# Optimization experiments

Measured on AMD Instinct MI355X. Metric: run time of the kernel, lower is better.

The kernel has to match this reference:

```python
import jax, jax.numpy as jnp
import numpy as np

N_NODES = 50000
N_EDGES = 1600000
NFEAT, NHID, NCLASS = 256, 128, 40
DROPOUT_P = 0.5


def gcn_conv(x, W, b, src, dst, n):
    # PyG GCNConv: h = X W; add self-loops; symmetric norm D^-1/2 (A+I) D^-1/2.
    h = x @ W  # [N, out]
    loop = jnp.arange(n, dtype=src.dtype)
    s = jnp.concatenate([src, loop])  # [E+N]
    d = jnp.concatenate([dst, loop])
    deg = jax.ops.segment_sum(jnp.ones_like(d, dtype=h.dtype), d, num_segments=n)  # in-degree incl. self-loop
    dinv = jax.lax.rsqrt(jnp.maximum(deg, 1.0))
    norm = dinv[s] * dinv[d]  # [E+N]
    msg = h[s] * norm[:, None]  # [E+N, out] gather
    out = jax.ops.segment_sum(msg, d, num_segments=n)  # scatter-add
    return out + b


def setup_inputs() -> dict:
    key = jax.random.key(0)
    k = jax.random.split(key, 7)
    x = jax.random.normal(k[0], (N_NODES, NFEAT), dtype=jnp.float32)
    edge_index = jax.random.randint(k[1], (2, N_EDGES), 0, N_NODES, dtype=jnp.int64)
    W1 = jax.random.normal(k[2], (NFEAT, NHID), dtype=jnp.float32) * (1.0 / np.sqrt(NFEAT))
    b1 = jnp.zeros((NHID,), dtype=jnp.float32)
    W2 = jax.random.normal(k[3], (NHID, NCLASS), dtype=jnp.float32) * (1.0 / np.sqrt(NHID))
    b2 = jnp.zeros((NCLASS,), dtype=jnp.float32)
    keep = jax.random.bernoulli(k[4], 1.0 - DROPOUT_P, (N_NODES, NHID))
    drop_mask = keep.astype(jnp.float32) / (1.0 - DROPOUT_P)  # fixed training-mode dropout mask
    return {"x": x, "edge_index": edge_index, "W1": W1, "b1": b1, "W2": W2, "b2": b2, "drop_mask": drop_mask}


def reference(x, edge_index, W1, b1, W2, b2, drop_mask):
    src, dst = edge_index[0], edge_index[1]
    h = gcn_conv(x, W1, b1, src, dst, N_NODES)
    h = jax.nn.relu(h)
    h = h * drop_mask  # F.dropout(training=True) with fixed mask
    h = gcn_conv(h, W2, b2, src, dst, N_NODES)
    return jax.nn.log_softmax(h, axis=1)
```

## Files before the change

kernel.cpp:

```cpp
#include <hip/hip_runtime.h>
#include <hip/hip_fp16.h>
#include <math.h>

#define N_NODES 50000
#define N_EDGES 1600000
#define NFEAT 256
#define NHID 128
#define NCLASS 40

#define BSHIFT 7
#define NBUCK 391
#define CAP 5120
#define EPB 4096

typedef _Float16 f16x8 __attribute__((ext_vector_type(8)));
typedef float f32x4 __attribute__((ext_vector_type(4)));

__global__ __launch_bounds__(256) void k_binA(const int* __restrict__ src,
                                              const int* __restrict__ dst,
                                              int* __restrict__ gcur,
                                              unsigned int* __restrict__ packed) {
    __shared__ int lhist[NBUCK];
    __shared__ int lbase[NBUCK];
    __shared__ int lcur[NBUCK];
    int t = threadIdx.x;
    for (int i = t; i < NBUCK; i += 256) { lhist[i] = 0; lcur[i] = 0; }
    __syncthreads();
    int e0 = blockIdx.x * EPB;
    int e1 = min(e0 + EPB, N_EDGES);
    for (int e = e0 + t; e < e1; e += 256) {
        int b = dst[e] >> BSHIFT;
        atomicAdd(&lhist[b], 1);
    }
    __syncthreads();
    for (int i = t; i < NBUCK; i += 256)
        lbase[i] = atomicAdd(&gcur[i], lhist[i]);
    __syncthreads();
    for (int e = e0 + t; e < e1; e += 256) {
        int d = dst[e];
        int b = d >> BSHIFT;
        int r = atomicAdd(&lcur[b], 1);
        int pos = lbase[b] + r;
        if (pos < CAP)
            packed[(size_t)b * CAP + pos] =
                ((unsigned int)src[e] << BSHIFT) | (unsigned int)(d & 127);
    }
}

__global__ __launch_bounds__(256) void k_binB(const int* __restrict__ gcur,
                                              const unsigned int* __restrict__ packed,
                                              int* __restrict__ esrc,
                                              int* __restrict__ row_beg,
                                              int* __restrict__ row_cnt,
                                              float* __restrict__ dinv) {
    __shared__ unsigned int sp[CAP];
    __shared__ int hist[128];
    __shared__ int scan[128];
    __shared__ int cur[128];
    int b = blockIdx.x;
    int t = threadIdx.x;
    int cnt = min(gcur[b], CAP);
    if (t < 128) { hist[t] = 0; cur[t] = 0; }
    __syncthreads();
    const unsigned int* pin = packed + (size_t)b * CAP;
    for (int i = t; i < cnt; i += 256) {
        unsigned int w = pin[i];
        sp[i] = w;
        atomicAdd(&hist[w & 127], 1);
    }
    __syncthreads();
    if (t == 0) {
        int s = 0;
        for (int i = 0; i < 128; i++) { scan[i] = s; s += hist[i]; }
    }
    __syncthreads();
    for (int i = t; i < cnt; i += 256) {
        unsigned int w = sp[i];
        int dl = (int)(w & 127u);
        int r = atomicAdd(&cur[dl], 1);
        esrc[(size_t)b * CAP + scan[dl] + r] = (int)(w >> BSHIFT);
    }
    if (t < 128) {
        int node = b * 128 + t;
        if (node < N_NODES) {
            row_beg[node] = b * CAP + scan[t];
            row_cnt[node] = hist[t];
            dinv[node] = rsqrtf((float)(hist[t] + 1));
        }
    }
}

__global__ __launch_bounds__(256) void k_prep(const float* __restrict__ W1,
                                              const float* __restrict__ W2,
                                              __half* __restrict__ w1t,
                                              __half* __restrict__ w2t,
                                              int* __restrict__ gcur) {
    int t = blockIdx.x * 256 + threadIdx.x;
    if (t < NBUCK) gcur[t] = 0;
    if (t < 128 * 256) {
        int n = t >> 8, k = t & 255;
        w1t[t] = __float2half(W1[k * NHID + n]);
    }
    if (t < 48 * 128) {
        int n = t >> 7, k = t & 127;
        w2t[t] = __float2half(n < NCLASS ? W2[k * NCLASS + n] : 0.0f);
    }
}

#define G1_LDA 72
#define G1_LDB 72
#define G1_LDE 136
__global__ __launch_bounds__(256) void k_gemm1(const float* __restrict__ x,
                                               const __half* __restrict__ w1t,
                                               __half* __restrict__ h1h) {
    __shared__ __half smem[64 * G1_LDA + 128 * G1_LDB];
    __half* sA = smem;
    __half* sB = smem + 64 * G1_LDA;
    int t = threadIdx.x;
    int rbase = blockIdx.x * 64;
    int lane = t & 63, wv = t >> 6;
    int m = lane & 15, quad = lane >> 4;
    f32x4 acc[8];
    #pragma unroll
    for (int i = 0; i < 8; i++) acc[i] = (f32x4)0.0f;

    int arow = t >> 2, aseg = t & 3;
    int grow = rbase + arow;
    bool avalid = grow < N_NODES;
    int bn = t >> 1, bseg = t & 1;

    for (int k0 = 0; k0 < NFEAT; k0 += 64) {
        const float4* gs = (const float4*)(x + (size_t)grow * NFEAT + k0 + aseg * 16);
        __half* ad = sA + arow * G1_LDA + aseg * 16;
        #pragma unroll
        for (int i = 0; i < 4; i++) {
            float4 v = avalid ? gs[i] : make_float4(0.f, 0.f, 0.f, 0.f);
            __half2 h0 = __float22half2_rn(make_float2(v.x, v.y));
            __half2 h1 = __float22half2_rn(make_float2(v.z, v.w));
            uint2 st;
            st.x = __builtin_bit_cast(unsigned int, h0);
            st.y = __builtin_bit_cast(unsigned int, h1);
            *(uint2*)(ad + i * 4) = st;
        }
        const uint4* ws4 = (const uint4*)(w1t + bn * NFEAT + k0 + bseg * 32);
        uint4* bd = (uint4*)(sB + bn * G1_LDB + bseg * 32);
        #pragma unroll
        for (int i = 0; i < 4; i++) bd[i] = ws4[i];
        __syncthreads();
        #pragma unroll
        for (int kk = 0; kk < 64; kk += 32) {
            f16x8 af = *(const f16x8*)(sA + (wv * 16 + m) * G1_LDA + kk + quad * 8);
            #pragma unroll
            for (int t8 = 0; t8 < 8; t8++) {
                f16x8 bf = *(const f16x8*)(sB + (t8 * 16 + m) * G1_LDB + kk + quad * 8);
                acc[t8] = __builtin_amdgcn_mfma_f32_16x16x32_f16(af, bf, acc[t8], 0, 0, 0);
            }
        }
        __syncthreads();
    }
    __half* eb = smem;
    #pragma unroll
    for (int t8 = 0; t8 < 8; t8++) {
        #pragma unroll
        for (int r = 0; r < 4; r++)
            eb[(wv * 16 + quad * 4 + r) * G1_LDE + t8 * 16 + m] = __float2half(acc[t8][r]);
    }
    __syncthreads();
    if (avalid) {
        const uint4* es = (const uint4*)(eb + arow * G1_LDE + aseg * 32);
        uint4* od = (uint4*)(h1h + (size_t)grow * NHID + aseg * 32);
        #pragma unroll
        for (int i = 0; i < 4; i++) od[i] = es[i];
    }
}

#define G2_LDA 136
#define G2_LDB 136
#define G2_LDE 72
__global__ __launch_bounds__(256) void k_gemm2(const __half* __restrict__ h1p,
                                               const __half* __restrict__ w2t,
                                               __half* __restrict__ h2p) {
    __shared__ __half smem[64 * G2_LDA + 48 * G2_LDB];
    __half* sA = smem;
    __half* sB = smem + 64 * G2_LDA;
    int t = threadIdx.x;
    int rbase = blockIdx.x * 64;
    int lane = t & 63, wv = t >> 6;
    int m = lane & 15, quad = lane >> 4;
    f32x4 acc[3];
    #pragma unroll
    for (int i = 0; i < 3; i++) acc[i] = (f32x4)0.0f;

    int arow = t >> 2, aseg = t & 3;
    int grow = rbase + arow;
    bool avalid = grow < N_NODES;

    #pragma unroll
    for (int i = 0; i < 3; i++) {
        int idx = t + i * 256;
        int n = idx >> 4, seg = idx & 15;
        *(uint4*)(sB + n * G2_LDB + seg * 8) = *(const uint4*)(w2t + n * NHID + seg * 8);
    }
    {
        const uint4* gs = (const uint4*)(h1p + (size_t)grow * NHID + aseg * 32);
        uint4* ad = (uint4*)(sA + arow * G2_LDA + aseg * 32);
        uint4 z; z.x = z.y = z.z = z.w = 0;
        #pragma unroll
        for (int i = 0; i < 4; i++) ad[i] = avalid ? gs[i] : z;
    }
    __syncthreads();
    #pragma unroll
    for (int kk = 0; kk < 128; kk += 32) {
        f16x8 af = *(const f16x8*)(sA + (wv * 16 + m) * G2_LDA + kk + quad * 8);
        #pragma unroll
        for (int t3 = 0; t3 < 3; t3++) {
            f16x8 bf = *(const f16x8*)(sB + (t3 * 16 + m) * G2_LDB + kk + quad * 8);
            acc[t3] = __builtin_amdgcn_mfma_f32_16x16x32_f16(af, bf, acc[t3], 0, 0, 0);
        }
    }
    __syncthreads();
    __half* eb = smem;
    #pragma unroll
    for (int t3 = 0; t3 < 3; t3++) {
        #pragma unroll
        for (int r = 0; r < 4; r++)
            eb[(wv * 16 + quad * 4 + r) * G2_LDE + t3 * 16 + m] = __float2half(acc[t3][r]);
    }
    {
        int zr = t >> 2, zc = 48 + (t & 3) * 4;
        uint2 z; z.x = z.y = 0;
        *(uint2*)(eb + zr * G2_LDE + zc) = z;
    }
    __syncthreads();
    #pragma unroll
    for (int i = 0; i < 2; i++) {
        int idx = t + i * 256;
        int row = idx >> 3, seg = idx & 7;
        int gr = rbase + row;
        if (gr < N_NODES)
            *(uint4*)(h2p + (size_t)gr * 64 + seg * 8) = *(const uint4*)(eb + row * G2_LDE + seg * 8);
    }
}

__device__ __forceinline__ void acc8f(float* acc, uint4 v, float d) {
    float2 a0 = __half22float2(__builtin_bit_cast(__half2, v.x));
    float2 a1 = __half22float2(__builtin_bit_cast(__half2, v.y));
    float2 a2 = __half22float2(__builtin_bit_cast(__half2, v.z));
    float2 a3 = __half22float2(__builtin_bit_cast(__half2, v.w));
    acc[0] = fmaf(a0.x, d, acc[0]); acc[1] = fmaf(a0.y, d, acc[1]);
    acc[2] = fmaf(a1.x, d, acc[2]); acc[3] = fmaf(a1.y, d, acc[3]);
    acc[4] = fmaf(a2.x, d, acc[4]); acc[5] = fmaf(a2.y, d, acc[5]);
    acc[6] = fmaf(a3.x, d, acc[6]); acc[7] = fmaf(a3.y, d, acc[7]);
}

__global__ __launch_bounds__(256, 8) void k_agg1(const __half* __restrict__ h1h,
                                                 const float* __restrict__ dinv,
                                                 const int* __restrict__ row_beg,
                                                 const int* __restrict__ row_cnt,
                                                 const int* __restrict__ esrc,
                                                 const float* __restrict__ b1,
                                                 const float* __restrict__ mask,
                                                 __half* __restrict__ h1p) {
    int i = blockIdx.x * 4 + (threadIdx.x >> 6);
    int lane = threadIdx.x & 63;
    int q = lane >> 4;
    int fl = lane & 15;
    const uint4* hv4 = (const uint4*)h1h;
    float di = dinv[i];
    __half2 hacc[4];
    __half2 hz = __half2half2(__float2half(0.0f));
    hacc[0] = hz; hacc[1] = hz; hacc[2] = hz; hacc[3] = hz;
    int s0 = row_beg[i], cnt = row_cnt[i];
    for (int base = 0; base < cnt; base += 64) {
        int idx = base + lane;
        int sv = (idx < cnt) ? esrc[s0 + idx] : 0;
        float dv = (idx < cnt) ? dinv[sv] : 0.0f;
        int n = min(64, cnt - base);
        int nr = (n + 31) & ~31;
        for (int j = 0; j < nr; j += 32) {
            int ss[8]; __half2 dd[8]; uint4 vv[8];
            #pragma unroll
            for (int k = 0; k < 8; k++) {
                int jx = j + 4 * k + q;
                ss[k] = __shfl(sv, jx);
                float df = __shfl(dv, jx);
                dd[k] = __half2half2(__float2half(df));
            }
            #pragma unroll
            for (int k = 0; k < 8; k++) vv[k] = hv4[(size_t)ss[k] * 16 + fl];
            #pragma unroll
            for (int k = 0; k < 8; k++) {
                hacc[0] = __hfma2(__builtin_bit_cast(__half2, vv[k].x), dd[k], hacc[0]);
                hacc[1] = __hfma2(__builtin_bit_cast(__half2, vv[k].y), dd[k], hacc[1]);
                hacc[2] = __hfma2(__builtin_bit_cast(__half2, vv[k].z), dd[k], hacc[2]);
                hacc[3] = __hfma2(__builtin_bit_cast(__half2, vv[k].w), dd[k], hacc[3]);
            }
        }
    }
    float acc[8];
    #pragma unroll
    for (int k2 = 0; k2 < 4; k2++) {
        float2 f = __half22float2(hacc[k2]);
        acc[2 * k2] = f.x; acc[2 * k2 + 1] = f.y;
    }
    #pragma unroll
    for (int k = 0; k < 8; k++) {
        acc[k] += __shfl_xor(acc[k], 16);
        acc[k] += __shfl_xor(acc[k], 32);
    }
    if (q == 0) {
        uint4 sv4 = hv4[(size_t)i * 16 + fl];
        acc8f(acc, sv4, di);
        float4 bb0 = ((const float4*)b1)[fl * 2];
        float4 bb1 = ((const float4*)b1)[fl * 2 + 1];
        const float4* mrow = (const float4*)(mask + (size_t)i * NHID);
        float4 mm0 = mrow[fl * 2];
        float4 mm1 = mrow[fl * 2 + 1];
        float o0 = fmaxf(fmaf(acc[0], di, bb0.x), 0.f) * mm0.x;
        float o1 = fmaxf(fmaf(acc[1], di, bb0.y), 0.f) * mm0.y;
        float o2 = fmaxf(fmaf(acc[2], di, bb0.z), 0.f) * mm0.z;
        float o3 = fmaxf(fmaf(acc[3], di, bb0.w), 0.f) * mm0.w;
        float o4 = fmaxf(fmaf(acc[4], di, bb1.x), 0.f) * mm1.x;
        float o5 = fmaxf(fmaf(acc[5], di, bb1.y), 0.f) * mm1.y;
        float o6 = fmaxf(fmaf(acc[6], di, bb1.z), 0.f) * mm1.z;
        float o7 = fmaxf(fmaf(acc[7], di, bb1.w), 0.f) * mm1.w;
        __half2 p0 = __float22half2_rn(make_float2(o0, o1));
        __half2 p1 = __float22half2_rn(make_float2(o2, o3));
        __half2 p2 = __float22half2_rn(make_float2(o4, o5));
        __half2 p3 = __float22half2_rn(make_float2(o6, o7));
        uint4 st;
        st.x = __builtin_bit_cast(unsigned int, p0);
        st.y = __builtin_bit_cast(unsigned int, p1);
        st.z = __builtin_bit_cast(unsigned int, p2);
        st.w = __builtin_bit_cast(unsigned int, p3);
        ((uint4*)h1p)[(size_t)i * 16 + fl] = st;
    }
}

__global__ __launch_bounds__(256, 8) void k_agg2(const __half* __restrict__ h2p,
                                                 const float* __restrict__ dinv,
                                                 const int* __restrict__ row_beg,
                                                 const int* __restrict__ row_cnt,
                                                 const int* __restrict__ esrc,
                                                 const float* __restrict__ b2,
                                                 float* __restrict__ out) {
    int i = blockIdx.x * 4 + (threadIdx.x >> 6);
    int lane = threadIdx.x & 63;
    int o8 = lane >> 3;
    int fl = lane & 7;
    const uint4* hv4 = (const uint4*)h2p;
    float di = dinv[i];
    __half2 hacc[4];
    __half2 hz = __half2half2(__float2half(0.0f));
    hacc[0] = hz; hacc[1] = hz; hacc[2] = hz; hacc[3] = hz;
    int s0 = row_beg[i], cnt = row_cnt[i];
    for (int base = 0; base < cnt; base += 64) {
        int idx = base + lane;
        int sv = (idx < cnt) ? esrc[s0 + idx] : 0;
        float dv = (idx < cnt) ? dinv[sv] : 0.0f;
        int n = min(64, cnt - base);
        int nr = (n + 31) & ~31;
        for (int j = 0; j < nr; j += 32) {
            int ss[4]; __half2 dd[4]; uint4 vv[4];
            #pragma unroll
            for (int k = 0; k < 4; k++) {
                int jx = j + 8 * k + o8;
                ss[k] = __shfl(sv, jx);
                float df = __shfl(dv, jx);
                dd[k] = __half2half2(__float2half(df));
            }
            #pragma unroll
            for (int k = 0; k < 4; k++) vv[k] = hv4[(size_t)ss[k] * 8 + fl];
            #pragma unroll
            for (int k = 0; k < 4; k++) {
                hacc[0] = __hfma2(__builtin_bit_cast(__half2, vv[k].x), dd[k], hacc[0]);
                hacc[1] = __hfma2(__builtin_bit_cast(__half2, vv[k].y), dd[k], hacc[1]);
                hacc[2] = __hfma2(__builtin_bit_cast(__half2, vv[k].z), dd[k], hacc[2]);
                hacc[3] = __hfma2(__builtin_bit_cast(__half2, vv[k].w), dd[k], hacc[3]);
            }
        }
    }
    float acc[8];
    #pragma unroll
    for (int k2 = 0; k2 < 4; k2++) {
        float2 f = __half22float2(hacc[k2]);
        acc[2 * k2] = f.x; acc[2 * k2 + 1] = f.y;
    }
    if (o8 == 0) {
        uint4 sv4 = hv4[(size_t)i * 8 + fl];
        acc8f(acc, sv4, di);
    }
    #pragma unroll
    for (int k = 0; k < 8; k++) {
        acc[k] += __shfl_xor(acc[k], 8);
        acc[k] += __shfl_xor(acc[k], 16);
        acc[k] += __shfl_xor(acc[k], 32);
    }
    if (o8 == 0) {
        bool act = (fl < 5);
        float val[8];
        float m = -INFINITY;
        if (act) {
            float4 bb0 = ((const float4*)b2)[fl * 2];
            float4 bb1 = ((const float4*)b2)[fl * 2 + 1];
            val[0] = fmaf(acc[0], di, bb0.x);
            val[1] = fmaf(acc[1], di, bb0.y);
            val[2] = fmaf(acc[2], di, bb0.z);
            val[3] = fmaf(acc[3], di, bb0.w);
            val[4] = fmaf(acc[4], di, bb1.x);
            val[5] = fmaf(acc[5], di, bb1.y);
            val[6] = fmaf(acc[6], di, bb1.z);
            val[7] = fmaf(acc[7], di, bb1.w);
            #pragma unroll
            for (int k = 0; k < 8; k++) m = fmaxf(m, val[k]);
        }
        m = fmaxf(m, __shfl_xor(m, 1));
        m = fmaxf(m, __shfl_xor(m, 2));
        m = fmaxf(m, __shfl_xor(m, 4));
        float ss = 0.f;
        if (act) {
            #pragma unroll
            for (int k = 0; k < 8; k++) ss += expf(val[k] - m);
        }
        ss += __shfl_xor(ss, 1);
        ss += __shfl_xor(ss, 2);
        ss += __shfl_xor(ss, 4);
        if (act) {
            float ls = m + logf(ss);
            float4 r0 = make_float4(val[0] - ls, val[1] - ls, val[2] - ls, val[3] - ls);
            float4 r1 = make_float4(val[4] - ls, val[5] - ls, val[6] - ls, val[7] - ls);
            float4* orow = (float4*)(out + (size_t)i * NCLASS + fl * 8);
            orow[0] = r0;
            orow[1] = r1;
        }
    }
}

extern "C" void kernel_launch(void* const* d_in, const int* in_sizes, int n_in,
                              void* d_out, int out_size, void* d_ws, size_t ws_size,
                              hipStream_t stream) {
    const float* x    = (const float*)d_in[0];
    const int*   ei   = (const int*)d_in[1];
    const float* W1   = (const float*)d_in[2];
    const float* b1   = (const float*)d_in[3];
    const float* W2   = (const float*)d_in[4];
    const float* b2   = (const float*)d_in[5];
    const float* mask = (const float*)d_in[6];
    float* out = (float*)d_out;

    const int* src = ei;
    const int* dst = ei + N_EDGES;

    char* ws = (char*)d_ws;
    size_t off = 0;
    __half* h1p    = (__half*)(ws + off); off += (size_t)N_NODES * NHID * 2;
    __half* h1h    = (__half*)(ws + off); off += (size_t)N_NODES * NHID * 2;
    int*    esrc   = (int*)   (ws + off); off += (size_t)NBUCK * CAP * 4;
    float*  dinv   = (float*) (ws + off); off += 200192;
    int*   row_beg = (int*)   (ws + off); off += 200192;
    int*   row_cnt = (int*)   (ws + off); off += 200192;
    int*   gcur    = (int*)   (ws + off); off += 2048;
    __half* w1t    = (__half*)(ws + off); off += 128 * 256 * 2;
    __half* w2t    = (__half*)(ws + off); off += 48 * 128 * 2;

    unsigned int* packed = (unsigned int*)h1p;
    __half* h2p = h1h;

    k_prep<<<128, 256, 0, stream>>>(W1, W2, w1t, w2t, gcur);
    k_binA<<<(N_EDGES + EPB - 1) / EPB, 256, 0, stream>>>(src, dst, gcur, packed);
    k_binB<<<NBUCK, 256, 0, stream>>>(gcur, packed, esrc, row_beg, row_cnt, dinv);

    k_gemm1<<<(N_NODES + 63) / 64, 256, 0, stream>>>(x, w1t, h1h);
    k_agg1<<<N_NODES / 4, 256, 0, stream>>>(h1h, dinv, row_beg, row_cnt, esrc, b1, mask, h1p);
    k_gemm2<<<(N_NODES + 63) / 64, 256, 0, stream>>>(h1p, w2t, h2p);
    k_agg2<<<N_NODES / 4, 256, 0, stream>>>(h2p, dinv, row_beg, row_cnt, esrc, b2, out);
}
```

Baseline: 269.5 us.

## Split hidden features into column planes so each aggregation pass gathers a cache-sized slice

The layer-1 features are written as four 32-column planes instead of 128-wide rows. The layer-1 aggregation now runs four times as many blocks, each gathering from one plane only, so the randomly accessed working set per pass is a quarter the size and more likely to stay in L2. Layer-2 features are stored as a 32-column plane plus an 8-column plane, dropping the zero padding to 64 columns and the writes of those padded columns. The trade-off is that edge indices and degree norms are re-read once per plane, and agg2 gains extra cross-lane reductions.

```diff
diff --git a/kernel.cpp b/kernel.cpp
--- a/kernel.cpp
+++ b/kernel.cpp
@@ -12,6 +12,9 @@
 #define NBUCK 391
 #define CAP 5120
 #define EPB 4096
+
+#define PL1 ((size_t)N_NODES * 32)
+#define PL2A ((size_t)N_NODES * 32)
 
 typedef _Float16 f16x8 __attribute__((ext_vector_type(8)));
 typedef float f32x4 __attribute__((ext_vector_type(4)));
@@ -168,7 +171,7 @@
     __syncthreads();
     if (avalid) {
         const uint4* es = (const uint4*)(eb + arow * G1_LDE + aseg * 32);
-        uint4* od = (uint4*)(h1h + (size_t)grow * NHID + aseg * 32);
+        uint4* od = (uint4*)(h1h + (size_t)aseg * PL1 + (size_t)grow * 32);
         #pragma unroll
         for (int i = 0; i < 4; i++) od[i] = es[i];
     }
@@ -226,19 +229,17 @@
         for (int r = 0; r < 4; r++)
             eb[(wv * 16 + quad * 4 + r) * G2_LDE + t3 * 16 + m] = __float2half(acc[t3][r]);
     }
-    {
-        int zr = t >> 2, zc = 48 + (t & 3) * 4;
-        uint2 z; z.x = z.y = 0;
-        *(uint2*)(eb + zr * G2_LDE + zc) = z;
-    }
     __syncthreads();
     #pragma unroll
     for (int i = 0; i < 2; i++) {
         int idx = t + i * 256;
         int row = idx >> 3, seg = idx & 7;
         int gr = rbase + row;
-        if (gr < N_NODES)
-            *(uint4*)(h2p + (size_t)gr * 64 + seg * 8) = *(const uint4*)(eb + row * G2_LDE + seg * 8);
+        if (gr < N_NODES && seg <= 4) {
+            uint4 v = *(const uint4*)(eb + row * G2_LDE + seg * 8);
+            if (seg < 4) ((uint4*)h2p)[(size_t)gr * 4 + seg] = v;
+            else        ((uint4*)(h2p + PL2A))[gr] = v;
+        }
     }
 }
 
@@ -261,11 +262,12 @@
                                                  const float* __restrict__ b1,
                                                  const float* __restrict__ mask,
                                                  __half* __restrict__ h1p) {
-    int i = blockIdx.x * 4 + (threadIdx.x >> 6);
+    int s = blockIdx.x / 12500;
+    int i = (blockIdx.x % 12500) * 4 + (threadIdx.x >> 6);
     int lane = threadIdx.x & 63;
-    int q = lane >> 4;
-    int fl = lane & 15;
-    const uint4* hv4 = (const uint4*)h1h;
+    int g = lane >> 2;
+    int fl = lane & 3;
+    const uint4* hp = (const uint4*)(h1h + (size_t)s * PL1);
     float di = dinv[i];
     __half2 hacc[4];
     __half2 hz = __half2half2(__float2half(0.0f));
@@ -275,47 +277,46 @@
         int idx = base + lane;
         int sv = (idx < cnt) ? esrc[s0 + idx] : 0;
         float dv = (idx < cnt) ? dinv[sv] : 0.0f;
-        int n = min(64, cnt - base);
-        int nr = (n + 31) & ~31;
-        for (int j = 0; j < nr; j += 32) {
-            int ss[8]; __half2 dd[8]; uint4 vv[8];
-            #pragma unroll
-            for (int k = 0; k < 8; k++) {
-                int jx = j + 4 * k + q;
-                ss[k] = __shfl(sv, jx);
-                float df = __shfl(dv, jx);
-                dd[k] = __half2half2(__float2half(df));
-            }
-            #pragma unroll
-            for (int k = 0; k < 8; k++) vv[k] = hv4[(size_t)ss[k] * 16 + fl];
-            #pragma unroll
-            for (int k = 0; k < 8; k++) {
-                hacc[0] = __hfma2(__builtin_bit_cast(__half2, vv[k].x), dd[k], hacc[0]);
-                hacc[1] = __hfma2(__builtin_bit_cast(__half2, vv[k].y), dd[k], hacc[1]);
-                hacc[2] = __hfma2(__builtin_bit_cast(__half2, vv[k].z), dd[k], hacc[2]);
-                hacc[3] = __hfma2(__builtin_bit_cast(__half2, vv[k].w), dd[k], hacc[3]);
-            }
-        }
-    }
-    float acc[8];
-    #pragma unroll
-    for (int k2 = 0; k2 < 4; k2++) {
-        float2 f = __half22float2(hacc[k2]);
-        acc[2 * k2] = f.x; acc[2 * k2 + 1] = f.y;
-    }
-    #pragma unroll
-    for (int k = 0; k < 8; k++) {
-        acc[k] += __shfl_xor(acc[k], 16);
-        acc[k] += __shfl_xor(acc[k], 32);
-    }
-    if (q == 0) {
-        uint4 sv4 = hv4[(size_t)i * 16 + fl];
+        int ss[4]; __half2 dd[4]; uint4 vv[4];
+        #pragma unroll
+        for (int k = 0; k < 4; k++) {
+            int jx = k * 16 + g;
+            ss[k] = __shfl(sv, jx);
+            dd[k] = __half2half2(__float2half(__shfl(dv, jx)));
+        }
+        #pragma unroll
+        for (int k = 0; k < 4; k++) vv[k] = hp[(size_t)ss[k] * 4 + fl];
+        #pragma unroll
+        for (int k = 0; k < 4; k++) {
+            hacc[0] = __hfma2(__builtin_bit_cast(__half2, vv[k].x), dd[k], hacc[0]);
+            hacc[1] = __hfma2(__builtin_bit_cast(__half2, vv[k].y), dd[k], hacc[1]);
+            hacc[2] = __hfma2(__builtin_bit_cast(__half2, vv[k].z), dd[k], hacc[2]);
+            hacc[3] = __hfma2(__builtin_bit_cast(__half2, vv[k].w), dd[k], hacc[3]);
+        }
+    }
+    #pragma unroll
+    for (int d = 4; d <= 32; d <<= 1) {
+        #pragma unroll
+        for (int r = 0; r < 4; r++) {
+            unsigned int u = __shfl_xor(__builtin_bit_cast(unsigned int, hacc[r]), d);
+            hacc[r] = __hadd2(hacc[r], __builtin_bit_cast(__half2, u));
+        }
+    }
+    if (g == 0) {
+        float acc[8];
+        #pragma unroll
+        for (int r = 0; r < 4; r++) {
+            float2 f = __half22float2(hacc[r]);
+            acc[2 * r] = f.x; acc[2 * r + 1] = f.y;
+        }
+        uint4 sv4 = hp[(size_t)i * 4 + fl];
         acc8f(acc, sv4, di);
-        float4 bb0 = ((const float4*)b1)[fl * 2];
-        float4 bb1 = ((const float4*)b1)[fl * 2 + 1];
-        const float4* mrow = (const float4*)(mask + (size_t)i * NHID);
-        float4 mm0 = mrow[fl * 2];
-        float4 mm1 = mrow[fl * 2 + 1];
+        const float4* bp = (const float4*)(b1 + s * 32 + fl * 8);
+        float4 bb0 = bp[0];
+        float4 bb1 = bp[1];
+        const float4* mrow = (const float4*)(mask + (size_t)i * NHID + s * 32 + fl * 8);
+        float4 mm0 = mrow[0];
+        float4 mm1 = mrow[1];
         float o0 = fmaxf(fmaf(acc[0], di, bb0.x), 0.f) * mm0.x;
         float o1 = fmaxf(fmaf(acc[1], di, bb0.y), 0.f) * mm0.y;
         float o2 = fmaxf(fmaf(acc[2], di, bb0.z), 0.f) * mm0.z;
@@ -333,7 +334,7 @@
         st.y = __builtin_bit_cast(unsigned int, p1);
         st.z = __builtin_bit_cast(unsigned int, p2);
         st.w = __builtin_bit_cast(unsigned int, p3);
-        ((uint4*)h1p)[(size_t)i * 16 + fl] = st;
+        ((uint4*)(h1p + (size_t)i * NHID + s * 32))[fl] = st;
     }
 }
 
@@ -346,92 +347,130 @@
                                                  float* __restrict__ out) {
     int i = blockIdx.x * 4 + (threadIdx.x >> 6);
     int lane = threadIdx.x & 63;
-    int o8 = lane >> 3;
-    int fl = lane & 7;
-    const uint4* hv4 = (const uint4*)h2p;
+    int g = lane >> 2;
+    int fl = lane & 3;
+    const uint4* hp0 = (const uint4*)h2p;
+    const uint4* hp1 = (const uint4*)(h2p + PL2A);
     float di = dinv[i];
-    __half2 hacc[4];
+    __half2 a0[4], a1[4];
     __half2 hz = __half2half2(__float2half(0.0f));
-    hacc[0] = hz; hacc[1] = hz; hacc[2] = hz; hacc[3] = hz;
+    #pragma unroll
+    for (int r = 0; r < 4; r++) { a0[r] = hz; a1[r] = hz; }
     int s0 = row_beg[i], cnt = row_cnt[i];
     for (int base = 0; base < cnt; base += 64) {
         int idx = base + lane;
         int sv = (idx < cnt) ? esrc[s0 + idx] : 0;
         float dv = (idx < cnt) ? dinv[sv] : 0.0f;
-        int n = min(64, cnt - base);
-        int nr = (n + 31) & ~31;
-        for (int j = 0; j < nr; j += 32) {
-            int ss[4]; __half2 dd[4]; uint4 vv[4];
-            #pragma unroll
-            for (int k = 0; k < 4; k++) {
-                int jx = j + 8 * k + o8;
-                ss[k] = __shfl(sv, jx);
-                float df = __shfl(dv, jx);
-                dd[k] = __half2half2(__float2half(df));
+        uint4 v1 = hp1[sv];
+        __half2 dvh = __half2half2(__float2half(dv));
+        a1[0] = __hfma2(__builtin_bit_cast(__half2, v1.x), dvh, a1[0]);
+        a1[1] = __hfma2(__builtin_bit_cast(__half2, v1.y), dvh, a1[1]);
+        a1[2] = __hfma2(__builtin_bit_cast(__half2, v1.z), dvh, a1[2]);
+        a1[3] = __hfma2(__builtin_bit_cast(__half2, v1.w), dvh, a1[3]);
+        int ss[4]; __half2 dd[4]; uint4 vv[4];
+        #pragma unroll
+        for (int k = 0; k < 4; k++) {
+            int jx = k * 16 + g;
+            ss[k] = __shfl(sv, jx);
+            dd[k] = __half2half2(__float2half(__shfl(dv, jx)));
+        }
+        #pragma unroll
+        for (int k = 0; k < 4; k++) vv[k] = hp0[(size_t)ss[k] * 4 + fl];
+        #pragma unroll
+        for (int k = 0; k < 4; k++) {
+            a0[0] = __hfma2(__builtin_bit_cast(__half2, vv[k].x), dd[k], a0[0]);
+            a0[1] = __hfma2(__builtin_bit_cast(__half2, vv[k].y), dd[k], a0[1]);
+            a0[2] = __hfma2(__builtin_bit_cast(__half2, vv[k].z), dd[k], a0[2]);
+            a0[3] = __hfma2(__builtin_bit_cast(__half2, vv[k].w), dd[k], a0[3]);
+        }
+    }
+    #pragma unroll
+    for (int d = 1; d <= 32; d <<= 1) {
+        #pragma unroll
+        for (int r = 0; r < 4; r++) {
+            unsigned int u = __shfl_xor(__builtin_bit_cast(unsigned int, a1[r]), d);
+            a1[r] = __hadd2(a1[r], __builtin_bit_cast(__half2, u));
+            if (d >= 4) {
+                unsigned int u0 = __shfl_xor(__builtin_bit_cast(unsigned int, a0[r]), d);
+                a0[r] = __hadd2(a0[r], __builtin_bit_cast(__half2, u0));
             }
-            #pragma unroll
-            for (int k = 0; k < 4; k++) vv[k] = hv4[(size_t)ss[k] * 8 + fl];
-            #pragma unroll
-            for (int k = 0; k < 4; k++) {
-                hacc[0] = __hfma2(__builtin_bit_cast(__half2, vv[k].x), dd[k], hacc[0]);
-                hacc[1] = __hfma2(__builtin_bit_cast(__half2, vv[k].y), dd[k], hacc[1]);
-                hacc[2] = __hfma2(__builtin_bit_cast(__half2, vv[k].z), dd[k], hacc[2]);
-                hacc[3] = __hfma2(__builtin_bit_cast(__half2, vv[k].w), dd[k], hacc[3]);
-            }
-        }
-    }
-    float acc[8];
-    #pragma unroll
-    for (int k2 = 0; k2 < 4; k2++) {
-        float2 f = __half22float2(hacc[k2]);
-        acc[2 * k2] = f.x; acc[2 * k2 + 1] = f.y;
-    }
-    if (o8 == 0) {
-        uint4 sv4 = hv4[(size_t)i * 8 + fl];
-        acc8f(acc, sv4, di);
-    }
-    #pragma unroll
-    for (int k = 0; k < 8; k++) {
-        acc[k] += __shfl_xor(acc[k], 8);
-        acc[k] += __shfl_xor(acc[k], 16);
-        acc[k] += __shfl_xor(acc[k], 32);
-    }
-    if (o8 == 0) {
-        bool act = (fl < 5);
-        float val[8];
-        float m = -INFINITY;
-        if (act) {
-            float4 bb0 = ((const float4*)b2)[fl * 2];
-            float4 bb1 = ((const float4*)b2)[fl * 2 + 1];
-            val[0] = fmaf(acc[0], di, bb0.x);
-            val[1] = fmaf(acc[1], di, bb0.y);
-            val[2] = fmaf(acc[2], di, bb0.z);
-            val[3] = fmaf(acc[3], di, bb0.w);
-            val[4] = fmaf(acc[4], di, bb1.x);
-            val[5] = fmaf(acc[5], di, bb1.y);
-            val[6] = fmaf(acc[6], di, bb1.z);
-            val[7] = fmaf(acc[7], di, bb1.w);
-            #pragma unroll
-            for (int k = 0; k < 8; k++) m = fmaxf(m, val[k]);
-        }
-        m = fmaxf(m, __shfl_xor(m, 1));
-        m = fmaxf(m, __shfl_xor(m, 2));
-        m = fmaxf(m, __shfl_xor(m, 4));
-        float ss = 0.f;
-        if (act) {
-            #pragma unroll
-            for (int k = 0; k < 8; k++) ss += expf(val[k] - m);
-        }
-        ss += __shfl_xor(ss, 1);
-        ss += __shfl_xor(ss, 2);
-        ss += __shfl_xor(ss, 4);
-        if (act) {
-            float ls = m + logf(ss);
-            float4 r0 = make_float4(val[0] - ls, val[1] - ls, val[2] - ls, val[3] - ls);
-            float4 r1 = make_float4(val[4] - ls, val[5] - ls, val[6] - ls, val[7] - ls);
-            float4* orow = (float4*)(out + (size_t)i * NCLASS + fl * 8);
-            orow[0] = r0;
-            orow[1] = r1;
+        }
+    }
+    float val0[8], val1[8];
+    if (g == 0) {
+        float acc[8];
+        #pragma unroll
+        for (int r = 0; r < 4; r++) {
+            float2 f = __half22float2(a0[r]);
+            acc[2 * r] = f.x; acc[2 * r + 1] = f.y;
+        }
+        uint4 s4 = hp0[(size_t)i * 4 + fl];
+        acc8f(acc, s4, di);
+        float4 bb0 = *(const float4*)(b2 + fl * 8);
+        float4 bb1 = *(const float4*)(b2 + fl * 8 + 4);
+        val0[0] = fmaf(acc[0], di, bb0.x);
+        val0[1] = fmaf(acc[1], di, bb0.y);
+        val0[2] = fmaf(acc[2], di, bb0.z);
+        val0[3] = fmaf(acc[3], di, bb0.w);
+        val0[4] = fmaf(acc[4], di, bb1.x);
+        val0[5] = fmaf(acc[5], di, bb1.y);
+        val0[6] = fmaf(acc[6], di, bb1.z);
+        val0[7] = fmaf(acc[7], di, bb1.w);
+    }
+    if (lane == 0) {
+        float acc[8];
+        #pragma unroll
+        for (int r = 0; r < 4; r++) {
+            float2 f = __half22float2(a1[r]);
+            acc[2 * r] = f.x; acc[2 * r + 1] = f.y;
+        }
+        acc8f(acc, hp1[i], di);
+        float4 bb0 = *(const float4*)(b2 + 32);
+        float4 bb1 = *(const float4*)(b2 + 36);
+        val1[0] = fmaf(acc[0], di, bb0.x);
+        val1[1] = fmaf(acc[1], di, bb0.y);
+        val1[2] = fmaf(acc[2], di, bb0.z);
+        val1[3] = fmaf(acc[3], di, bb0.w);
+        val1[4] = fmaf(acc[4], di, bb1.x);
+        val1[5] = fmaf(acc[5], di, bb1.y);
+        val1[6] = fmaf(acc[6], di, bb1.z);
+        val1[7] = fmaf(acc[7], di, bb1.w);
+    }
+    float m = -INFINITY;
+    if (g == 0) {
+        #pragma unroll
+        for (int k = 0; k < 8; k++) m = fmaxf(m, val0[k]);
+    }
+    if (lane == 0) {
+        #pragma unroll
+        for (int k = 0; k < 8; k++) m = fmaxf(m, val1[k]);
+    }
+    m = fmaxf(m, __shfl_xor(m, 1));
+    m = fmaxf(m, __shfl_xor(m, 2));
+    float ssum = 0.f;
+    if (g == 0) {
+        #pragma unroll
+        for (int k = 0; k < 8; k++) ssum += expf(val0[k] - m);
+    }
+    if (lane == 0) {
+        #pragma unroll
+        for (int k = 0; k < 8; k++) ssum += expf(val1[k] - m);
+    }
+    ssum += __shfl_xor(ssum, 1);
+    ssum += __shfl_xor(ssum, 2);
+    if (g == 0) {
+        float ls = m + logf(ssum);
+        float4 r0 = make_float4(val0[0] - ls, val0[1] - ls, val0[2] - ls, val0[3] - ls);
+        float4 r1 = make_float4(val0[4] - ls, val0[5] - ls, val0[6] - ls, val0[7] - ls);
+        float4* orow = (float4*)(out + (size_t)i * NCLASS + fl * 8);
+        orow[0] = r0;
+        orow[1] = r1;
+        if (lane == 0) {
+            float4 r2 = make_float4(val1[0] - ls, val1[1] - ls, val1[2] - ls, val1[3] - ls);
+            float4 r3 = make_float4(val1[4] - ls, val1[5] - ls, val1[6] - ls, val1[7] - ls);
+            float4* orow1 = (float4*)(out + (size_t)i * NCLASS + 32);
+            orow1[0] = r2;
+            orow1[1] = r3;
         }
     }
 }
@@ -471,7 +510,7 @@
     k_binB<<<NBUCK, 256, 0, stream>>>(gcur, packed, esrc, row_beg, row_cnt, dinv);
 
     k_gemm1<<<(N_NODES + 63) / 64, 256, 0, stream>>>(x, w1t, h1h);
-    k_agg1<<<N_NODES / 4, 256, 0, stream>>>(h1h, dinv, row_beg, row_cnt, esrc, b1, mask, h1p);
+    k_agg1<<<50000, 256, 0, stream>>>(h1h, dinv, row_beg, row_cnt, esrc, b1, mask, h1p);
     k_gemm2<<<(N_NODES + 63) / 64, 256, 0, stream>>>(h1p, w2t, h2p);
-    k_agg2<<<N_NODES / 4, 256, 0, stream>>>(h2p, dinv, row_beg, row_cnt, esrc, b2, out);
-}
+    k_agg2<<<12500, 256, 0, stream>>>(h2p, dinv, row_beg, row_cnt, esrc, b2, out);
+}
```

After: 332.9 us. 23.5% more time.

## Fold source-node normalization into GEMM epilogues and use padded dummy row in aggregation

Applied to the files above, without the earlier changes.

Each GEMM epilogue now multiplies its output rows by dinv of that row, so the aggregation kernels only sum gathered rows instead of loading dinv[src] per edge and doing FMAs. The aggregation loops drop the shuffle-based broadcast of edge indices. Each lane loads its edge indices directly, and out-of-range slots point to a zero-scaled dummy padded row, which removes branching. Buffers are padded to NPAD rows and dinv is zeroed for the padding rows. The trade-off is more redundant esrc loads per lane and unconditional writes to the padded rows.

```diff
diff --git a/kernel.cpp b/kernel.cpp
--- a/kernel.cpp
+++ b/kernel.cpp
@@ -7,6 +7,9 @@
 #define NFEAT 256
 #define NHID 128
 #define NCLASS 40
+
+#define NPAD 50048
+#define DUMMY N_NODES
 
 #define BSHIFT 7
 #define NBUCK 391
@@ -94,7 +97,8 @@
                                               const float* __restrict__ W2,
                                               __half* __restrict__ w1t,
                                               __half* __restrict__ w2t,
-                                              int* __restrict__ gcur) {
+                                              int* __restrict__ gcur,
+                                              float* __restrict__ dinv) {
     int t = blockIdx.x * 256 + threadIdx.x;
     if (t < NBUCK) gcur[t] = 0;
     if (t < 128 * 256) {
@@ -105,6 +109,7 @@
         int n = t >> 7, k = t & 127;
         w2t[t] = __float2half(n < NCLASS ? W2[k * NCLASS + n] : 0.0f);
     }
+    if (t >= N_NODES && t < NPAD) dinv[t] = 0.0f;
 }
 
 #define G1_LDA 72
@@ -112,6 +117,7 @@
 #define G1_LDE 136
 __global__ __launch_bounds__(256) void k_gemm1(const float* __restrict__ x,
                                                const __half* __restrict__ w1t,
+                                               const float* __restrict__ dinv,
                                                __half* __restrict__ h1h) {
     __shared__ __half smem[64 * G1_LDA + 128 * G1_LDB];
     __half* sA = smem;
@@ -158,15 +164,18 @@
         }
         __syncthreads();
     }
+    float di4[4];
+    #pragma unroll
+    for (int r = 0; r < 4; r++) di4[r] = dinv[rbase + wv * 16 + quad * 4 + r];
     __half* eb = smem;
     #pragma unroll
     for (int t8 = 0; t8 < 8; t8++) {
         #pragma unroll
         for (int r = 0; r < 4; r++)
-            eb[(wv * 16 + quad * 4 + r) * G1_LDE + t8 * 16 + m] = __float2half(acc[t8][r]);
-    }
-    __syncthreads();
-    if (avalid) {
+            eb[(wv * 16 + quad * 4 + r) * G1_LDE + t8 * 16 + m] = __float2half(acc[t8][r] * di4[r]);
+    }
+    __syncthreads();
+    {
         const uint4* es = (const uint4*)(eb + arow * G1_LDE + aseg * 32);
         uint4* od = (uint4*)(h1h + (size_t)grow * NHID + aseg * 32);
         #pragma unroll
@@ -179,6 +188,7 @@
 #define G2_LDE 72
 __global__ __launch_bounds__(256) void k_gemm2(const __half* __restrict__ h1p,
                                                const __half* __restrict__ w2t,
+                                               const float* __restrict__ dinv,
                                                __half* __restrict__ h2p) {
     __shared__ __half smem[64 * G2_LDA + 48 * G2_LDB];
     __half* sA = smem;
@@ -219,12 +229,15 @@
         }
     }
     __syncthreads();
+    float di4[4];
+    #pragma unroll
+    for (int r = 0; r < 4; r++) di4[r] = dinv[rbase + wv * 16 + quad * 4 + r];
     __half* eb = smem;
     #pragma unroll
     for (int t3 = 0; t3 < 3; t3++) {
         #pragma unroll
         for (int r = 0; r < 4; r++)
-            eb[(wv * 16 + quad * 4 + r) * G2_LDE + t3 * 16 + m] = __float2half(acc[t3][r]);
+            eb[(wv * 16 + quad * 4 + r) * G2_LDE + t3 * 16 + m] = __float2half(acc[t3][r] * di4[r]);
     }
     {
         int zr = t >> 2, zc = 48 + (t & 3) * 4;
@@ -237,8 +250,7 @@
         int idx = t + i * 256;
         int row = idx >> 3, seg = idx & 7;
         int gr = rbase + row;
-        if (gr < N_NODES)
-            *(uint4*)(h2p + (size_t)gr * 64 + seg * 8) = *(const uint4*)(eb + row * G2_LDE + seg * 8);
+        *(uint4*)(h2p + (size_t)gr * 64 + seg * 8) = *(const uint4*)(eb + row * G2_LDE + seg * 8);
     }
 }
 
@@ -263,7 +275,7 @@
                                                  __half* __restrict__ h1p) {
     int i = blockIdx.x * 4 + (threadIdx.x >> 6);
     int lane = threadIdx.x & 63;
-    int q = lane >> 4;
+    int g = lane >> 4;
     int fl = lane & 15;
     const uint4* hv4 = (const uint4*)h1h;
     float di = dinv[i];
@@ -271,46 +283,46 @@
     __half2 hz = __half2half2(__float2half(0.0f));
     hacc[0] = hz; hacc[1] = hz; hacc[2] = hz; hacc[3] = hz;
     int s0 = row_beg[i], cnt = row_cnt[i];
+    unsigned cm1 = (unsigned)(cnt - 1);
     for (int base = 0; base < cnt; base += 64) {
-        int idx = base + lane;
-        int sv = (idx < cnt) ? esrc[s0 + idx] : 0;
-        float dv = (idx < cnt) ? dinv[sv] : 0.0f;
-        int n = min(64, cnt - base);
-        int nr = (n + 31) & ~31;
-        for (int j = 0; j < nr; j += 32) {
-            int ss[8]; __half2 dd[8]; uint4 vv[8];
+        #pragma unroll
+        for (int h = 0; h < 2; h++) {
+            int e8[8]; uint4 vv[8];
             #pragma unroll
             for (int k = 0; k < 8; k++) {
-                int jx = j + 4 * k + q;
-                ss[k] = __shfl(sv, jx);
-                float df = __shfl(dv, jx);
-                dd[k] = __half2half2(__float2half(df));
+                int jx = base + (h * 8 + k) * 4 + g;
+                unsigned li = min((unsigned)jx, cm1);
+                int e = esrc[s0 + (int)li];
+                e8[k] = (jx < cnt) ? e : DUMMY;
             }
             #pragma unroll
-            for (int k = 0; k < 8; k++) vv[k] = hv4[(size_t)ss[k] * 16 + fl];
+            for (int k = 0; k < 8; k++) vv[k] = hv4[(size_t)e8[k] * 16 + fl];
             #pragma unroll
             for (int k = 0; k < 8; k++) {
-                hacc[0] = __hfma2(__builtin_bit_cast(__half2, vv[k].x), dd[k], hacc[0]);
-                hacc[1] = __hfma2(__builtin_bit_cast(__half2, vv[k].y), dd[k], hacc[1]);
-                hacc[2] = __hfma2(__builtin_bit_cast(__half2, vv[k].z), dd[k], hacc[2]);
-                hacc[3] = __hfma2(__builtin_bit_cast(__half2, vv[k].w), dd[k], hacc[3]);
+                hacc[0] = __hadd2(hacc[0], __builtin_bit_cast(__half2, vv[k].x));
+                hacc[1] = __hadd2(hacc[1], __builtin_bit_cast(__half2, vv[k].y));
+                hacc[2] = __hadd2(hacc[2], __builtin_bit_cast(__half2, vv[k].z));
+                hacc[3] = __hadd2(hacc[3], __builtin_bit_cast(__half2, vv[k].w));
             }
         }
     }
-    float acc[8];
-    #pragma unroll
-    for (int k2 = 0; k2 < 4; k2++) {
-        float2 f = __half22float2(hacc[k2]);
-        acc[2 * k2] = f.x; acc[2 * k2 + 1] = f.y;
-    }
-    #pragma unroll
-    for (int k = 0; k < 8; k++) {
-        acc[k] += __shfl_xor(acc[k], 16);
-        acc[k] += __shfl_xor(acc[k], 32);
-    }
-    if (q == 0) {
+    #pragma unroll
+    for (int d = 16; d <= 32; d <<= 1) {
+        #pragma unroll
+        for (int r = 0; r < 4; r++) {
+            unsigned int u = __shfl_xor(__builtin_bit_cast(unsigned int, hacc[r]), d);
+            hacc[r] = __hadd2(hacc[r], __builtin_bit_cast(__half2, u));
+        }
+    }
+    if (g == 0) {
+        float acc[8];
+        #pragma unroll
+        for (int r = 0; r < 4; r++) {
+            float2 f = __half22float2(hacc[r]);
+            acc[2 * r] = f.x; acc[2 * r + 1] = f.y;
+        }
         uint4 sv4 = hv4[(size_t)i * 16 + fl];
-        acc8f(acc, sv4, di);
+        acc8f(acc, sv4, 1.0f);
         float4 bb0 = ((const float4*)b1)[fl * 2];
         float4 bb1 = ((const float4*)b1)[fl * 2 + 1];
         const float4* mrow = (const float4*)(mask + (size_t)i * NHID);
@@ -346,7 +358,7 @@
                                                  float* __restrict__ out) {
     int i = blockIdx.x * 4 + (threadIdx.x >> 6);
     int lane = threadIdx.x & 63;
-    int o8 = lane >> 3;
+    int g = lane >> 3;
     int fl = lane & 7;
     const uint4* hv4 = (const uint4*)h2p;
     float di = dinv[i];
@@ -354,50 +366,44 @@
     __half2 hz = __half2half2(__float2half(0.0f));
     hacc[0] = hz; hacc[1] = hz; hacc[2] = hz; hacc[3] = hz;
     int s0 = row_beg[i], cnt = row_cnt[i];
+    unsigned cm1 = (unsigned)(cnt - 1);
     for (int base = 0; base < cnt; base += 64) {
-        int idx = base + lane;
-        int sv = (idx < cnt) ? esrc[s0 + idx] : 0;
-        float dv = (idx < cnt) ? dinv[sv] : 0.0f;
-        int n = min(64, cnt - base);
-        int nr = (n + 31) & ~31;
-        for (int j = 0; j < nr; j += 32) {
-            int ss[4]; __half2 dd[4]; uint4 vv[4];
-            #pragma unroll
-            for (int k = 0; k < 4; k++) {
-                int jx = j + 8 * k + o8;
-                ss[k] = __shfl(sv, jx);
-                float df = __shfl(dv, jx);
-                dd[k] = __half2half2(__float2half(df));
-            }
-            #pragma unroll
-            for (int k = 0; k < 4; k++) vv[k] = hv4[(size_t)ss[k] * 8 + fl];
-            #pragma unroll
-            for (int k = 0; k < 4; k++) {
-                hacc[0] = __hfma2(__builtin_bit_cast(__half2, vv[k].x), dd[k], hacc[0]);
-                hacc[1] = __hfma2(__builtin_bit_cast(__half2, vv[k].y), dd[k], hacc[1]);
-                hacc[2] = __hfma2(__builtin_bit_cast(__half2, vv[k].z), dd[k], hacc[2]);
-                hacc[3] = __hfma2(__builtin_bit_cast(__half2, vv[k].w), dd[k], hacc[3]);
-            }
-        }
-    }
-    float acc[8];
-    #pragma unroll
-    for (int k2 = 0; k2 < 4; k2++) {
-        float2 f = __half22float2(hacc[k2]);
-        acc[2 * k2] = f.x; acc[2 * k2 + 1] = f.y;
-    }
-    if (o8 == 0) {
+        int e8[8]; uint4 vv[8];
+        #pragma unroll
+        for (int k = 0; k < 8; k++) {
+            int jx = base + k * 8 + g;
+            unsigned li = min((unsigned)jx, cm1);
+            int e = esrc[s0 + (int)li];
+            e8[k] = (jx < cnt) ? e : DUMMY;
+        }
+        #pragma unroll
+        for (int k = 0; k < 8; k++) vv[k] = hv4[(size_t)e8[k] * 8 + fl];
+        #pragma unroll
+        for (int k = 0; k < 8; k++) {
+            hacc[0] = __hadd2(hacc[0], __builtin_bit_cast(__half2, vv[k].x));
+            hacc[1] = __hadd2(hacc[1], __builtin_bit_cast(__half2, vv[k].y));
+            hacc[2] = __hadd2(hacc[2], __builtin_bit_cast(__half2, vv[k].z));
+            hacc[3] = __hadd2(hacc[3], __builtin_bit_cast(__half2, vv[k].w));
+        }
+    }
+    #pragma unroll
+    for (int d = 8; d <= 32; d <<= 1) {
+        #pragma unroll
+        for (int r = 0; r < 4; r++) {
+            unsigned int u = __shfl_xor(__builtin_bit_cast(unsigned int, hacc[r]), d);
+            hacc[r] = __hadd2(hacc[r], __builtin_bit_cast(__half2, u));
+        }
+    }
+    if (g == 0) {
+        bool act = (fl < 5);
+        float acc[8];
+        #pragma unroll
+        for (int r = 0; r < 4; r++) {
+            float2 f = __half22float2(hacc[r]);
+            acc[2 * r] = f.x; acc[2 * r + 1] = f.y;
+        }
         uint4 sv4 = hv4[(size_t)i * 8 + fl];
-        acc8f(acc, sv4, di);
-    }
-    #pragma unroll
-    for (int k = 0; k < 8; k++) {
-        acc[k] += __shfl_xor(acc[k], 8);
-        acc[k] += __shfl_xor(acc[k], 16);
-        acc[k] += __shfl_xor(acc[k], 32);
-    }
-    if (o8 == 0) {
-        bool act = (fl < 5);
+        acc8f(acc, sv4, 1.0f);
         float val[8];
         float m = -INFINITY;
         if (act) {
@@ -453,9 +459,9 @@
 
     char* ws = (char*)d_ws;
     size_t off = 0;
-    __half* h1p    = (__half*)(ws + off); off += (size_t)N_NODES * NHID * 2;
-    __half* h1h    = (__half*)(ws + off); off += (size_t)N_NODES * NHID * 2;
-    int*    esrc   = (int*)   (ws + off); off += (size_t)NBUCK * CAP * 4;
+    __half* h1p    = (__half*)(ws + off); off += (size_t)NPAD * NHID * 2;
+    __half* h1h    = (__half*)(ws + off); off += (size_t)NPAD * NHID * 2;
+    int*    esrc   = (int*)   (ws + off); off += (size_t)NBUCK * CAP * 4 + 256;
     float*  dinv   = (float*) (ws + off); off += 200192;
     int*   row_beg = (int*)   (ws + off); off += 200192;
     int*   row_cnt = (int*)   (ws + off); off += 200192;
@@ -466,12 +472,12 @@
     unsigned int* packed = (unsigned int*)h1p;
     __half* h2p = h1h;
 
-    k_prep<<<128, 256, 0, stream>>>(W1, W2, w1t, w2t, gcur);
+    k_prep<<<196, 256, 0, stream>>>(W1, W2, w1t, w2t, gcur, dinv);
     k_binA<<<(N_EDGES + EPB - 1) / EPB, 256, 0, stream>>>(src, dst, gcur, packed);
     k_binB<<<NBUCK, 256, 0, stream>>>(gcur, packed, esrc, row_beg, row_cnt, dinv);
 
-    k_gemm1<<<(N_NODES + 63) / 64, 256, 0, stream>>>(x, w1t, h1h);
+    k_gemm1<<<NPAD / 64, 256, 0, stream>>>(x, w1t, dinv, h1h);
     k_agg1<<<N_NODES / 4, 256, 0, stream>>>(h1h, dinv, row_beg, row_cnt, esrc, b1, mask, h1p);
-    k_gemm2<<<(N_NODES + 63) / 64, 256, 0, stream>>>(h1p, w2t, h2p);
+    k_gemm2<<<NPAD / 64, 256, 0, stream>>>(h1p, w2t, dinv, h2p);
     k_agg2<<<N_NODES / 4, 256, 0, stream>>>(h2p, dinv, row_beg, row_cnt, esrc, b2, out);
 }
```

After: 278.9 us. 3.5% more time.
